# Performance work log

Hardware: AMD Instinct MI355X
Metric: run time of the kernel (lower is better)

Reference implementation:

```python
import jax, jax.numpy as jnp
import numpy as np

B, T, IN, PRE, LH, NH, ACT_H, NPOL, NVAL = 32, 512, 256, 512, 512, 1024, 512, 64, 1


def setup_inputs() -> dict:
    key = jax.random.key(0)
    ks = jax.random.split(key, 10)
    def w(k, shape, fan_in):
        return jax.random.normal(k, shape, jnp.float32) / np.sqrt(fan_in).astype(np.float32)
    return {
        "x": jax.random.normal(ks[0], (B, T, IN), jnp.float32),
        "pre_W0": w(ks[1], (PRE, IN), IN), "pre_b0": jnp.zeros((PRE,), jnp.float32),
        "pre_W1": w(ks[2], (LH, PRE), PRE), "pre_b1": jnp.zeros((LH,), jnp.float32),
        "weight_ih": w(ks[3], (4 * NH, LH), LH), "weight_hh": w(ks[4], (4 * NH, NH), NH),
        "bias_ih": jnp.zeros((4 * NH,), jnp.float32), "bias_hh": jnp.zeros((4 * NH,), jnp.float32),
        "act_W0": w(ks[5], (ACT_H, NH), NH), "act_b0": jnp.zeros((ACT_H,), jnp.float32),
        "act_W1": w(ks[6], (NPOL, ACT_H), ACT_H), "act_b1": jnp.zeros((NPOL,), jnp.float32),
        "val_W0": w(ks[7], (ACT_H, NH), NH), "val_b0": jnp.zeros((ACT_H,), jnp.float32),
        "val_W1": w(ks[8], (NVAL, ACT_H), ACT_H), "val_b1": jnp.zeros((NVAL,), jnp.float32),
    }


def reference(x, pre_W0, pre_b0, pre_W1, pre_b1, weight_ih, weight_hh, bias_ih, bias_hh,
              act_W0, act_b0, act_W1, act_b1, val_W0, val_b0, val_W1, val_b1):
    # pre_dnn: relu hidden layer + linear output ('linear')
    h = jnp.maximum(x @ pre_W0.T + pre_b0, 0.0)
    u = h @ pre_W1.T + pre_b1                         # [B,T,LH]
    # SeqLSTM: torch lstm_cell semantics (gate order i,f,g,o), zero initial (h,c)
    # precompute input contribution to gates outside the scan
    x_gates = u @ weight_ih.T + (bias_ih + bias_hh)   # [B,T,4H]
    x_gates = jnp.swapaxes(x_gates, 0, 1)             # [T,B,4H]
    H = weight_hh.shape[1]

    def step(carry, gx):
        hh, cc = carry
        gates = gx + hh @ weight_hh.T
        i, f, g, o = jnp.split(gates, 4, axis=-1)
        cc = jax.nn.sigmoid(f) * cc + jax.nn.sigmoid(i) * jnp.tanh(g)
        hh = jax.nn.sigmoid(o) * jnp.tanh(cc)
        return (hh, cc), hh

    init = (jnp.zeros((x.shape[0], H), x.dtype), jnp.zeros((x.shape[0], H), x.dtype))
    _, hs = jax.lax.scan(step, init, x_gates)         # hs: [T,B,H]
    hs = jnp.swapaxes(hs, 0, 1)                       # [B,T,H]
    # act_dnn ('softmax') and val_dnn ('linear') on all hidden states
    a = jnp.maximum(hs @ act_W0.T + act_b0, 0.0)
    probs = jax.nn.softmax(a @ act_W1.T + act_b1, axis=-1)   # [B,T,NPOL]
    v = jnp.maximum(hs @ val_W0.T + val_b0, 0.0)
    value = v @ val_W1.T + val_b1                              # [B,T,NVAL]
    return probs, value
```

## Files before the change

### kernel.cpp

```cpp
#include <hip/hip_runtime.h>
#include <stdint.h>

#define TT 512
#define NB 32

typedef __attribute__((ext_vector_type(8))) short bf16x8;
typedef __attribute__((ext_vector_type(4))) float f32x4;

#define O_XB   0ull
#define O_W0   8388608ull
#define O_W1   8650752ull
#define O_WIH  9175040ull
#define O_WHH  13369344ull
#define O_WA0  21757952ull
#define O_WA1  22806528ull
#define O_WV0  22872064ull
#define O_WV1  23920640ull
#define O_GB   23921664ull
#define O_H1   23938048ull
#define O_U    40715264ull
#define O_GX   57492480ull
#define O_HS   191710208ull
#define O_HBUF 225264640ull
#define O_FLG  225395712ull
#define WS_NEED 225399808ull

__device__ __forceinline__ unsigned short f2bf(float f) {
  unsigned u = __builtin_bit_cast(unsigned, f);
  u = (u + 0x7fffu + ((u >> 16) & 1u)) >> 16;
  return (unsigned short)u;
}
__device__ __forceinline__ float bf2f(unsigned short h) {
  unsigned u = ((unsigned)h) << 16;
  return __builtin_bit_cast(float, u);
}
__device__ __forceinline__ float bf2f_lo(unsigned w) { return __builtin_bit_cast(float, w << 16); }
__device__ __forceinline__ float bf2f_hi(unsigned w) { return __builtin_bit_cast(float, w & 0xffff0000u); }

__device__ __forceinline__ float dot8(uint4 a, uint4 b, float acc) {
  acc = fmaf(bf2f_lo(a.x), bf2f_lo(b.x), acc);
  acc = fmaf(bf2f_hi(a.x), bf2f_hi(b.x), acc);
  acc = fmaf(bf2f_lo(a.y), bf2f_lo(b.y), acc);
  acc = fmaf(bf2f_hi(a.y), bf2f_hi(b.y), acc);
  acc = fmaf(bf2f_lo(a.z), bf2f_lo(b.z), acc);
  acc = fmaf(bf2f_hi(a.z), bf2f_hi(b.z), acc);
  acc = fmaf(bf2f_lo(a.w), bf2f_lo(b.w), acc);
  acc = fmaf(bf2f_hi(a.w), bf2f_hi(b.w), acc);
  return acc;
}
__device__ __forceinline__ float sigf(float x) { return 1.f / (1.f + __expf(-x)); }
__device__ __forceinline__ float tanhf_(float x) { float e = __expf(2.f * x); return 1.f - 2.f / (e + 1.f); }

__global__ void cvt_kernel(const float* __restrict__ x,  const float* __restrict__ w0,
                           const float* __restrict__ w1, const float* __restrict__ wih,
                           const float* __restrict__ whh, const float* __restrict__ wa0,
                           const float* __restrict__ wa1, const float* __restrict__ wv0,
                           const float* __restrict__ wv1, const float* __restrict__ bih,
                           const float* __restrict__ bhh, unsigned char* __restrict__ ws) {
  unsigned i = blockIdx.x * 256u + threadIdx.x;
  if (i >= 2991232u) return;
  const float* s; unsigned long long off; unsigned local;
  if      (i < 1048576u) { s = x;   off = O_XB;  local = i; }
  else if (i < 1081344u) { s = w0;  off = O_W0;  local = i - 1048576u; }
  else if (i < 1146880u) { s = w1;  off = O_W1;  local = i - 1081344u; }
  else if (i < 1671168u) { s = wih; off = O_WIH; local = i - 1146880u; }
  else if (i < 2719744u) { s = whh; off = O_WHH; local = i - 1671168u; }
  else if (i < 2850816u) { s = wa0; off = O_WA0; local = i - 2719744u; }
  else if (i < 2859008u) { s = wa1; off = O_WA1; local = i - 2850816u; }
  else if (i < 2990080u) { s = wv0; off = O_WV0; local = i - 2859008u; }
  else if (i < 2990208u) { s = wv1; off = O_WV1; local = i - 2990080u; }
  else {
    unsigned l2 = i - 2990208u;
    float4 a = ((const float4*)bih)[l2];
    float4 b = ((const float4*)bhh)[l2];
    float4 o; o.x = a.x + b.x; o.y = a.y + b.y; o.z = a.z + b.z; o.w = a.w + b.w;
    ((float4*)(ws + O_GB))[l2] = o;
    return;
  }
  float4 v = ((const float4*)s)[local];
  ushort4 o; o.x = f2bf(v.x); o.y = f2bf(v.y); o.z = f2bf(v.z); o.w = f2bf(v.w);
  ((ushort4*)(ws + off))[local] = o;
}

template<int RELU, int ILV>
__global__ __launch_bounds__(256, 2) void gemm_bt(const unsigned short* __restrict__ A,
    const unsigned short* __restrict__ Bw, const float* __restrict__ bias,
    unsigned short* __restrict__ C, int M, int N, int K) {
  __shared__ unsigned short As[128 * 40];
  __shared__ unsigned short Bs[128 * 40];
  const int tid = threadIdx.x;
  const int l = tid & 63, w = tid >> 6;
  const int wm = (w >> 1) * 64, wn = (w & 1) * 64;
  const int m0 = blockIdx.y * 128, n0 = blockIdx.x * 128;
  const int sr = tid >> 2;
  const int sk = (tid & 3) * 8;
  const int fr = l & 15;
  const int kf = (l >> 4) * 8;
  f32x4 acc[4][4] = {};
  for (int kb = 0; kb < K; kb += 32) {
    uint4 a0 = *(const uint4*)(A + (size_t)(m0 + sr) * K + kb + sk);
    uint4 a1 = *(const uint4*)(A + (size_t)(m0 + sr + 64) * K + kb + sk);
    uint4 b0 = *(const uint4*)(Bw + (size_t)(n0 + sr) * K + kb + sk);
    uint4 b1 = *(const uint4*)(Bw + (size_t)(n0 + sr + 64) * K + kb + sk);
    __syncthreads();
    *(uint4*)(As + sr * 40 + sk) = a0;
    *(uint4*)(As + (sr + 64) * 40 + sk) = a1;
    *(uint4*)(Bs + sr * 40 + sk) = b0;
    *(uint4*)(Bs + (sr + 64) * 40 + sk) = b1;
    __syncthreads();
    bf16x8 af[4], bfr[4];
    #pragma unroll
    for (int mt = 0; mt < 4; mt++)
      af[mt] = __builtin_bit_cast(bf16x8, *(const uint4*)(As + (wm + mt * 16 + fr) * 40 + kf));
    #pragma unroll
    for (int nt = 0; nt < 4; nt++)
      bfr[nt] = __builtin_bit_cast(bf16x8, *(const uint4*)(Bs + (wn + nt * 16 + fr) * 40 + kf));
    #pragma unroll
    for (int mt = 0; mt < 4; mt++)
      #pragma unroll
      for (int nt = 0; nt < 4; nt++)
        acc[mt][nt] = __builtin_amdgcn_mfma_f32_16x16x32_bf16(af[mt], bfr[nt], acc[mt][nt], 0, 0, 0);
  }
  const int rq = (l >> 4) * 4;
  #pragma unroll
  for (int nt = 0; nt < 4; nt++) {
    int n = n0 + wn + nt * 16 + fr;
    float bv = bias[n];
    #pragma unroll
    for (int mt = 0; mt < 4; mt++) {
      int rb = m0 + wm + mt * 16 + rq;
      #pragma unroll
      for (int i = 0; i < 4; i++) {
        float v = acc[mt][nt][i] + bv;
        if (RELU) v = fmaxf(v, 0.f);
        int r = rb + i;
        size_t orow = ILV ? ((size_t)(r & (TT - 1)) * NB + (size_t)(r >> 9)) : (size_t)r;
        C[orow * (size_t)N + n] = f2bf(v);
      }
    }
  }
}

__global__ __launch_bounds__(256, 1) void lstm_scan(
    const unsigned short* __restrict__ whh,
    const unsigned short* __restrict__ gx,
    unsigned short* __restrict__ hbuf,
    unsigned short* __restrict__ hs,
    unsigned int* __restrict__ flags) {
  __shared__ float part[4096];
  const int tid = threadIdx.x;
  const int l = tid & 63, w = tid >> 6;
  const int g = blockIdx.x >> 6;
  const int s = blockIdx.x & 63;
  const int fr = l & 15, kf = (l >> 4) * 8;

  bf16x8 wf[4][8];
  #pragma unroll
  for (int q = 0; q < 4; q++)
    #pragma unroll
    for (int ks = 0; ks < 8; ks++) {
      int row = q * 1024 + s * 16 + fr;
      int k = w * 256 + ks * 32 + kf;
      wf[q][ks] = __builtin_bit_cast(bf16x8, *(const uint4*)(whh + (size_t)row * 1024 + k));
    }

  const int pm = tid >> 3;
  const int j2 = (tid & 7) * 2;
  float c0 = 0.f, c1 = 0.f;
  unsigned int* myflag = flags + (size_t)(g * 64 + s) * 8;
  const unsigned int* pollp = flags + (size_t)(g * 64 + l) * 8;

  for (int t = 0; t < TT; t++) {
    unsigned gxw0 = 0, gxw1 = 0, gxw2 = 0, gxw3 = 0;
    if (tid < 128) {
      const unsigned* gp = (const unsigned*)(gx + ((size_t)t * NB + g * 16 + pm) * 4096 + s * 16 + j2);
      gxw0 = gp[0]; gxw1 = gp[512]; gxw2 = gp[1024]; gxw3 = gp[1536];
    }
    if (t > 0 && w == 0) {
      while (true) {
        unsigned f = __hip_atomic_load(pollp, __ATOMIC_RELAXED, __HIP_MEMORY_SCOPE_AGENT);
        if (!__any((int)(f < (unsigned)t))) break;
        __builtin_amdgcn_s_sleep(1);
      }
    }
    __syncthreads();
    asm volatile("" ::: "memory");

    const unsigned short* hb = hbuf + (size_t)(g * 2 + (t & 1)) * 16384;
    const unsigned long long* hq = (const unsigned long long*)(hb + (size_t)fr * 1024);
    bf16x8 hf[8];
    #pragma unroll
    for (int ks = 0; ks < 8; ks++) {
      int k4 = (w * 256 + ks * 32 + kf) >> 2;
      unsigned long long lo = __hip_atomic_load(hq + k4,     __ATOMIC_RELAXED, __HIP_MEMORY_SCOPE_AGENT);
      unsigned long long hi = __hip_atomic_load(hq + k4 + 1, __ATOMIC_RELAXED, __HIP_MEMORY_SCOPE_AGENT);
      uint4 u; u.x = (unsigned)lo; u.y = (unsigned)(lo >> 32);
      u.z = (unsigned)hi; u.w = (unsigned)(hi >> 32);
      hf[ks] = __builtin_bit_cast(bf16x8, u);
    }
    f32x4 acc[4] = {};
    #pragma unroll
    for (int ks = 0; ks < 8; ks++)
      #pragma unroll
      for (int q = 0; q < 4; q++)
        acc[q] = __builtin_amdgcn_mfma_f32_16x16x32_bf16(hf[ks], wf[q][ks], acc[q], 0, 0, 0);
    #pragma unroll
    for (int q = 0; q < 4; q++)
      *(f32x4*)(&part[((w * 4 + q) * 64 + l) * 4]) = acc[q];
    __syncthreads();

    if (tid < 128) {
      const int lane0 = (pm >> 2) * 16 + j2;
      const int reg = pm & 3;
      unsigned gxw[4] = {gxw0, gxw1, gxw2, gxw3};
      float gv[4][2];
      #pragma unroll
      for (int q = 0; q < 4; q++) {
        float v0 = bf2f_lo(gxw[q]);
        float v1 = bf2f_hi(gxw[q]);
        #pragma unroll
        for (int ww = 0; ww < 4; ww++) {
          v0 += part[((ww * 4 + q) * 64 + lane0) * 4 + reg];
          v1 += part[((ww * 4 + q) * 64 + lane0 + 1) * 4 + reg];
        }
        gv[q][0] = v0; gv[q][1] = v1;
      }
      float si0 = sigf(gv[0][0]), si1 = sigf(gv[0][1]);
      float sf0 = sigf(gv[1][0]), sf1 = sigf(gv[1][1]);
      float tg0 = tanhf_(gv[2][0]), tg1 = tanhf_(gv[2][1]);
      float so0 = sigf(gv[3][0]), so1 = sigf(gv[3][1]);
      c0 = sf0 * c0 + si0 * tg0;
      c1 = sf1 * c1 + si1 * tg1;
      float h0 = so0 * tanhf_(c0);
      float h1 = so1 * tanhf_(c1);
      unsigned hv = (unsigned)f2bf(h0) | ((unsigned)f2bf(h1) << 16);
      unsigned short* hn = hbuf + (size_t)(g * 2 + ((t + 1) & 1)) * 16384;
      __hip_atomic_store((unsigned*)(hn + (size_t)pm * 1024 + s * 16 + j2), hv,
                         __ATOMIC_RELAXED, __HIP_MEMORY_SCOPE_AGENT);
      *(unsigned*)(hs + ((size_t)(g * 16 + pm) * TT + t) * 1024 + s * 16 + j2) = hv;
      asm volatile("s_waitcnt vmcnt(0)" ::: "memory");
    }
    __syncthreads();
    if (tid == 0)
      __hip_atomic_store(myflag, (unsigned)(t + 1), __ATOMIC_RELAXED, __HIP_MEMORY_SCOPE_AGENT);
  }
}

__global__ __launch_bounds__(512, 1) void act1_softmax(const unsigned short* __restrict__ Aa,
    const unsigned short* __restrict__ W1, const float* __restrict__ b1,
    float* __restrict__ out) {
  __shared__ unsigned short wl[64 * 512];
  const int tid = threadIdx.x;
  #pragma unroll
  for (int r = 0; r < 8; r++) {
    int e = r * 512 + tid;
    int col = e >> 6, kc = e & 63;
    *(uint4*)(wl + ((size_t)kc * 64 + col) * 8) = *(const uint4*)(W1 + (size_t)col * 512 + kc * 8);
  }
  __syncthreads();
  const int l = tid & 63, w = tid >> 6;
  size_t row = (size_t)blockIdx.x * 8 + w;
  const unsigned short* ar = Aa + row * 512;
  float acc = 0.f;
  for (int kc = 0; kc < 64; kc++) {
    uint4 au = *(const uint4*)(ar + kc * 8);
    uint4 wu = *(const uint4*)(wl + ((size_t)kc * 64 + l) * 8);
    acc = dot8(au, wu, acc);
  }
  float logit = acc + b1[l];
  float mx = logit;
  #pragma unroll
  for (int off = 32; off >= 1; off >>= 1) mx = fmaxf(mx, __shfl_xor(mx, off));
  float e = __expf(logit - mx);
  float ssum = e;
  #pragma unroll
  for (int off = 32; off >= 1; off >>= 1) ssum += __shfl_xor(ssum, off);
  out[row * 64 + l] = e / ssum;
}

__global__ __launch_bounds__(256, 4) void val1_kernel(const unsigned short* __restrict__ V,
    const unsigned short* __restrict__ w1, const float* __restrict__ b1,
    float* __restrict__ out) {
  const int tid = threadIdx.x;
  const int l = tid & 63, w = tid >> 6;
  size_t row = (size_t)blockIdx.x * 4 + w;
  uint4 vu = *(const uint4*)(V + row * 512 + l * 8);
  uint4 wu = *(const uint4*)(w1 + l * 8);
  float s = dot8(vu, wu, 0.f);
  #pragma unroll
  for (int off = 32; off >= 1; off >>= 1) s += __shfl_xor(s, off);
  if (l == 0) out[1048576u + row] = s + b1[0];
}

extern "C" void kernel_launch(void* const* d_in, const int* in_sizes, int n_in,
                              void* d_out, int out_size, void* d_ws, size_t ws_size,
                              hipStream_t stream) {
  (void)in_sizes; (void)n_in; (void)out_size;
  if (ws_size < WS_NEED) return;
  const float* x   = (const float*)d_in[0];
  const float* pw0 = (const float*)d_in[1];
  const float* pb0 = (const float*)d_in[2];
  const float* pw1 = (const float*)d_in[3];
  const float* pb1 = (const float*)d_in[4];
  const float* wih = (const float*)d_in[5];
  const float* whh = (const float*)d_in[6];
  const float* bih = (const float*)d_in[7];
  const float* bhh = (const float*)d_in[8];
  const float* aw0 = (const float*)d_in[9];
  const float* ab0 = (const float*)d_in[10];
  const float* aw1 = (const float*)d_in[11];
  const float* ab1 = (const float*)d_in[12];
  const float* vw0 = (const float*)d_in[13];
  const float* vb0 = (const float*)d_in[14];
  const float* vw1 = (const float*)d_in[15];
  const float* vb1 = (const float*)d_in[16];
  unsigned char* ws = (unsigned char*)d_ws;
  float* out = (float*)d_out;

  const unsigned short* xb   = (const unsigned short*)(ws + O_XB);
  const unsigned short* w0b  = (const unsigned short*)(ws + O_W0);
  const unsigned short* w1b  = (const unsigned short*)(ws + O_W1);
  const unsigned short* wihb = (const unsigned short*)(ws + O_WIH);
  const unsigned short* whhb = (const unsigned short*)(ws + O_WHH);
  const unsigned short* wa0b = (const unsigned short*)(ws + O_WA0);
  const unsigned short* wa1b = (const unsigned short*)(ws + O_WA1);
  const unsigned short* wv0b = (const unsigned short*)(ws + O_WV0);
  const unsigned short* wv1b = (const unsigned short*)(ws + O_WV1);
  const float* gbp = (const float*)(ws + O_GB);
  unsigned short* h1b = (unsigned short*)(ws + O_H1);
  unsigned short* ub  = (unsigned short*)(ws + O_U);
  unsigned short* gxb = (unsigned short*)(ws + O_GX);
  unsigned short* hsb = (unsigned short*)(ws + O_HS);
  unsigned short* hbufp = (unsigned short*)(ws + O_HBUF);
  unsigned int* flgp = (unsigned int*)(ws + O_FLG);
  unsigned short* aab = h1b;
  unsigned short* vvb = ub;

  hipMemsetAsync(ws + O_HBUF, 0, 131072 + 4096, stream);
  cvt_kernel<<<11685, 256, 0, stream>>>(x, pw0, pw1, wih, whh, aw0, aw1, vw0, vw1, bih, bhh, ws);
  gemm_bt<1, 0><<<dim3(4, 128), 256, 0, stream>>>(xb, w0b, pb0, h1b, 16384, 512, 256);
  gemm_bt<0, 0><<<dim3(4, 128), 256, 0, stream>>>(h1b, w1b, pb1, ub, 16384, 512, 512);
  gemm_bt<0, 1><<<dim3(32, 128), 256, 0, stream>>>(ub, wihb, gbp, gxb, 16384, 4096, 512);
  {
    const unsigned short* a_whh = whhb;
    const unsigned short* a_gx  = gxb;
    unsigned short* a_hbuf = hbufp;
    unsigned short* a_hs   = hsb;
    unsigned int*   a_flg  = flgp;
    void* args[5] = { (void*)&a_whh, (void*)&a_gx, (void*)&a_hbuf, (void*)&a_hs, (void*)&a_flg };
    hipLaunchCooperativeKernel((void*)lstm_scan, dim3(128), dim3(256), args, 0, stream);
  }
  gemm_bt<1, 0><<<dim3(4, 128), 256, 0, stream>>>(hsb, wa0b, ab0, aab, 16384, 512, 1024);
  gemm_bt<1, 0><<<dim3(4, 128), 256, 0, stream>>>(hsb, wv0b, vb0, vvb, 16384, 512, 1024);
  act1_softmax<<<2048, 512, 0, stream>>>(aab, wa1b, ab1, out);
  val1_kernel<<<4096, 256, 0, stream>>>(vvb, wv1b, vb1, out);
}
```

Before: 2.530 ms.

## Replace per-block flags with step-tagged hidden-state packets in LSTM scan

The recurrent scan no longer uses per-block flag words polled by one wave followed by barriers. Each bf16 hidden value is now stored in a 32-bit word whose upper half carries the timestep tag. Consumers spin on the data itself until every tag matches, so the flag store, the vmcnt wait and one block barrier per step go away. The cost is twice the bytes for hidden-state exchange and every wave polling its own data. The buffer is also moved into the reused H1 region, with the memset placed after the GEMMs.

New measurement: 4.464 ms. +76.4%, slower.

```diff
diff --git a/kernel.cpp b/kernel.cpp
--- a/kernel.cpp
+++ b/kernel.cpp
@@ -21,18 +21,12 @@
 #define O_U    40715264ull
 #define O_GX   57492480ull
 #define O_HS   191710208ull
-#define O_HBUF 225264640ull
-#define O_FLG  225395712ull
-#define WS_NEED 225399808ull
+#define WS_NEED 225264640ull
 
 __device__ __forceinline__ unsigned short f2bf(float f) {
   unsigned u = __builtin_bit_cast(unsigned, f);
   u = (u + 0x7fffu + ((u >> 16) & 1u)) >> 16;
   return (unsigned short)u;
-}
-__device__ __forceinline__ float bf2f(unsigned short h) {
-  unsigned u = ((unsigned)h) << 16;
-  return __builtin_bit_cast(float, u);
 }
 __device__ __forceinline__ float bf2f_lo(unsigned w) { return __builtin_bit_cast(float, w << 16); }
 __device__ __forceinline__ float bf2f_hi(unsigned w) { return __builtin_bit_cast(float, w & 0xffff0000u); }
@@ -144,9 +138,8 @@
 __global__ __launch_bounds__(256, 1) void lstm_scan(
     const unsigned short* __restrict__ whh,
     const unsigned short* __restrict__ gx,
-    unsigned short* __restrict__ hbuf,
-    unsigned short* __restrict__ hs,
-    unsigned int* __restrict__ flags) {
+    unsigned* __restrict__ pk,
+    unsigned short* __restrict__ hs) {
   __shared__ float part[4096];
   const int tid = threadIdx.x;
   const int l = tid & 63, w = tid >> 6;
@@ -166,9 +159,8 @@
 
   const int pm = tid >> 3;
   const int j2 = (tid & 7) * 2;
+  const int kh = w * 128 + (kf >> 1);
   float c0 = 0.f, c1 = 0.f;
-  unsigned int* myflag = flags + (size_t)(g * 64 + s) * 8;
-  const unsigned int* pollp = flags + (size_t)(g * 64 + l) * 8;
 
   for (int t = 0; t < TT; t++) {
     unsigned gxw0 = 0, gxw1 = 0, gxw2 = 0, gxw3 = 0;
@@ -176,27 +168,38 @@
       const unsigned* gp = (const unsigned*)(gx + ((size_t)t * NB + g * 16 + pm) * 4096 + s * 16 + j2);
       gxw0 = gp[0]; gxw1 = gp[512]; gxw2 = gp[1024]; gxw3 = gp[1536];
     }
-    if (t > 0 && w == 0) {
-      while (true) {
-        unsigned f = __hip_atomic_load(pollp, __ATOMIC_RELAXED, __HIP_MEMORY_SCOPE_AGENT);
-        if (!__any((int)(f < (unsigned)t))) break;
-        __builtin_amdgcn_s_sleep(1);
+
+    const unsigned long long* hq =
+        (const unsigned long long*)(pk + (((size_t)(g * 2 + (t & 1)) * 16 + fr) << 10));
+    unsigned long long raw[32];
+    const unsigned expv = ((unsigned)t) << 16;
+    while (true) {
+      #pragma unroll
+      for (int ks = 0; ks < 8; ks++)
+        #pragma unroll
+        for (int j = 0; j < 4; j++)
+          raw[ks * 4 + j] = __hip_atomic_load(hq + kh + ks * 16 + j,
+                                              __ATOMIC_RELAXED, __HIP_MEMORY_SCOPE_AGENT);
+      unsigned mism = 0;
+      #pragma unroll
+      for (int i = 0; i < 32; i++) {
+        unsigned lo = (unsigned)raw[i];
+        unsigned hi = (unsigned)(raw[i] >> 32);
+        mism |= ((lo ^ expv) | (hi ^ expv)) & 0xffff0000u;
       }
-    }
-    __syncthreads();
-    asm volatile("" ::: "memory");
-
-    const unsigned short* hb = hbuf + (size_t)(g * 2 + (t & 1)) * 16384;
-    const unsigned long long* hq = (const unsigned long long*)(hb + (size_t)fr * 1024);
+      if (!__any((int)(mism != 0u))) break;
+      __builtin_amdgcn_s_sleep(1);
+    }
+
     bf16x8 hf[8];
     #pragma unroll
     for (int ks = 0; ks < 8; ks++) {
-      int k4 = (w * 256 + ks * 32 + kf) >> 2;
-      unsigned long long lo = __hip_atomic_load(hq + k4,     __ATOMIC_RELAXED, __HIP_MEMORY_SCOPE_AGENT);
-      unsigned long long hi = __hip_atomic_load(hq + k4 + 1, __ATOMIC_RELAXED, __HIP_MEMORY_SCOPE_AGENT);
-      uint4 u; u.x = (unsigned)lo; u.y = (unsigned)(lo >> 32);
-      u.z = (unsigned)hi; u.w = (unsigned)(hi >> 32);
-      hf[ks] = __builtin_bit_cast(bf16x8, u);
+      #pragma unroll
+      for (int j = 0; j < 4; j++) {
+        unsigned long long r_ = raw[ks * 4 + j];
+        hf[ks][2 * j]     = (short)(unsigned short)(r_ & 0xffffu);
+        hf[ks][2 * j + 1] = (short)(unsigned short)((r_ >> 32) & 0xffffu);
+      }
     }
     f32x4 acc[4] = {};
     #pragma unroll
@@ -204,6 +207,7 @@
       #pragma unroll
       for (int q = 0; q < 4; q++)
         acc[q] = __builtin_amdgcn_mfma_f32_16x16x32_bf16(hf[ks], wf[q][ks], acc[q], 0, 0, 0);
+    __syncthreads();
     #pragma unroll
     for (int q = 0; q < 4; q++)
       *(f32x4*)(&part[((w * 4 + q) * 64 + l) * 4]) = acc[q];
@@ -233,16 +237,16 @@
       c1 = sf1 * c1 + si1 * tg1;
       float h0 = so0 * tanhf_(c0);
       float h1 = so1 * tanhf_(c1);
-      unsigned hv = (unsigned)f2bf(h0) | ((unsigned)f2bf(h1) << 16);
-      unsigned short* hn = hbuf + (size_t)(g * 2 + ((t + 1) & 1)) * 16384;
-      __hip_atomic_store((unsigned*)(hn + (size_t)pm * 1024 + s * 16 + j2), hv,
-                         __ATOMIC_RELAXED, __HIP_MEMORY_SCOPE_AGENT);
-      *(unsigned*)(hs + ((size_t)(g * 16 + pm) * TT + t) * 1024 + s * 16 + j2) = hv;
-      asm volatile("s_waitcnt vmcnt(0)" ::: "memory");
-    }
-    __syncthreads();
-    if (tid == 0)
-      __hip_atomic_store(myflag, (unsigned)(t + 1), __ATOMIC_RELAXED, __HIP_MEMORY_SCOPE_AGENT);
+      unsigned hb0 = (unsigned)f2bf(h0), hb1 = (unsigned)f2bf(h1);
+      unsigned tagw = ((unsigned)(t + 1)) << 16;
+      unsigned long long pkt = (unsigned long long)(hb0 | tagw) |
+                               ((unsigned long long)(hb1 | tagw) << 32);
+      unsigned long long* dst = (unsigned long long*)(
+          pk + (((size_t)(g * 2 + ((t + 1) & 1)) * 16 + pm) << 10) + s * 16 + j2);
+      __hip_atomic_store(dst, pkt, __ATOMIC_RELAXED, __HIP_MEMORY_SCOPE_AGENT);
+      *(unsigned*)(hs + ((size_t)(g * 16 + pm) * TT + t) * 1024 + s * 16 + j2) =
+          hb0 | (hb1 << 16);
+    }
   }
 }
 
@@ -331,23 +335,21 @@
   unsigned short* ub  = (unsigned short*)(ws + O_U);
   unsigned short* gxb = (unsigned short*)(ws + O_GX);
   unsigned short* hsb = (unsigned short*)(ws + O_HS);
-  unsigned short* hbufp = (unsigned short*)(ws + O_HBUF);
-  unsigned int* flgp = (unsigned int*)(ws + O_FLG);
+  unsigned* pkb = (unsigned*)(ws + O_H1);
   unsigned short* aab = h1b;
   unsigned short* vvb = ub;
 
-  hipMemsetAsync(ws + O_HBUF, 0, 131072 + 4096, stream);
   cvt_kernel<<<11685, 256, 0, stream>>>(x, pw0, pw1, wih, whh, aw0, aw1, vw0, vw1, bih, bhh, ws);
   gemm_bt<1, 0><<<dim3(4, 128), 256, 0, stream>>>(xb, w0b, pb0, h1b, 16384, 512, 256);
   gemm_bt<0, 0><<<dim3(4, 128), 256, 0, stream>>>(h1b, w1b, pb1, ub, 16384, 512, 512);
   gemm_bt<0, 1><<<dim3(32, 128), 256, 0, stream>>>(ub, wihb, gbp, gxb, 16384, 4096, 512);
+  hipMemsetAsync(ws + O_H1, 0, 4 * 16 * 1024 * 4, stream);
   {
     const unsigned short* a_whh = whhb;
     const unsigned short* a_gx  = gxb;
-    unsigned short* a_hbuf = hbufp;
-    unsigned short* a_hs   = hsb;
-    unsigned int*   a_flg  = flgp;
-    void* args[5] = { (void*)&a_whh, (void*)&a_gx, (void*)&a_hbuf, (void*)&a_hs, (void*)&a_flg };
+    unsigned*       a_pk = pkb;
+    unsigned short* a_hs = hsb;
+    void* args[4] = { (void*)&a_whh, (void*)&a_gx, (void*)&a_pk, (void*)&a_hs };
     hipLaunchCooperativeKernel((void*)lstm_scan, dim3(128), dim3(256), args, 0, stream);
   }
   gemm_bt<1, 0><<<dim3(4, 128), 256, 0, stream>>>(hsb, wa0b, ab0, aab, 16384, 512, 1024);
```

## Store LSTM hidden state in MFMA fragment order and defer hs write

Applied to the files above, without the earlier changes.

The exchange buffer for h between scan blocks is rearranged into the MFMA operand fragment layout, so each lane reads its fragment with contiguous coalesced 16-byte loads instead of strided row reads. The hs history store is moved after the flag publish, taking it off the critical path of the per-step barrier. The h buffer and flags now reuse the dead h1 workspace region, cleared just before the scan. This requires more complex index math on the producer side and relies on the h1 region being unused while the scan runs.

Measured after the change: 2.350 ms. -7.1%, faster.

```diff
diff --git a/kernel.cpp b/kernel.cpp
--- a/kernel.cpp
+++ b/kernel.cpp
@@ -21,18 +21,12 @@
 #define O_U    40715264ull
 #define O_GX   57492480ull
 #define O_HS   191710208ull
-#define O_HBUF 225264640ull
-#define O_FLG  225395712ull
-#define WS_NEED 225399808ull
+#define WS_NEED 225264640ull
 
 __device__ __forceinline__ unsigned short f2bf(float f) {
   unsigned u = __builtin_bit_cast(unsigned, f);
   u = (u + 0x7fffu + ((u >> 16) & 1u)) >> 16;
   return (unsigned short)u;
-}
-__device__ __forceinline__ float bf2f(unsigned short h) {
-  unsigned u = ((unsigned)h) << 16;
-  return __builtin_bit_cast(float, u);
 }
 __device__ __forceinline__ float bf2f_lo(unsigned w) { return __builtin_bit_cast(float, w << 16); }
 __device__ __forceinline__ float bf2f_hi(unsigned w) { return __builtin_bit_cast(float, w & 0xffff0000u); }
@@ -144,9 +138,8 @@
 __global__ __launch_bounds__(256, 1) void lstm_scan(
     const unsigned short* __restrict__ whh,
     const unsigned short* __restrict__ gx,
-    unsigned short* __restrict__ hbuf,
-    unsigned short* __restrict__ hs,
-    unsigned int* __restrict__ flags) {
+    unsigned* __restrict__ pk,
+    unsigned short* __restrict__ hs) {
   __shared__ float part[4096];
   const int tid = threadIdx.x;
   const int l = tid & 63, w = tid >> 6;
@@ -166,9 +159,18 @@
 
   const int pm = tid >> 3;
   const int j2 = (tid & 7) * 2;
+  const int D0  = s * 16 + j2;
+  const int pw  = D0 >> 8;
+  const int pr  = D0 & 255;
+  const int pks = pr >> 5;
+  const int pkfg= (pr & 31) >> 3;
+  const int pjj = (pr & 7) >> 1;
+  const unsigned pidx = ((unsigned)((pw * 8 + pks) * 64 + pkfg * 16 + pm) << 2) + pjj;
+
+  unsigned* flags = pk + 32768;
+  unsigned* myflag = flags + (size_t)(g * 64 + s) * 8;
+  const unsigned* pollp = flags + (size_t)(g * 64 + l) * 8;
   float c0 = 0.f, c1 = 0.f;
-  unsigned int* myflag = flags + (size_t)(g * 64 + s) * 8;
-  const unsigned int* pollp = flags + (size_t)(g * 64 + l) * 8;
 
   for (int t = 0; t < TT; t++) {
     unsigned gxw0 = 0, gxw1 = 0, gxw2 = 0, gxw3 = 0;
@@ -186,14 +188,14 @@
     __syncthreads();
     asm volatile("" ::: "memory");
 
-    const unsigned short* hb = hbuf + (size_t)(g * 2 + (t & 1)) * 16384;
-    const unsigned long long* hq = (const unsigned long long*)(hb + (size_t)fr * 1024);
+    const unsigned long long* hq =
+        (const unsigned long long*)(pk + (size_t)(g * 2 + (t & 1)) * 8192);
     bf16x8 hf[8];
     #pragma unroll
     for (int ks = 0; ks < 8; ks++) {
-      int k4 = (w * 256 + ks * 32 + kf) >> 2;
-      unsigned long long lo = __hip_atomic_load(hq + k4,     __ATOMIC_RELAXED, __HIP_MEMORY_SCOPE_AGENT);
-      unsigned long long hi = __hip_atomic_load(hq + k4 + 1, __ATOMIC_RELAXED, __HIP_MEMORY_SCOPE_AGENT);
+      size_t i2 = ((size_t)(w * 8 + ks) * 64 + l) * 2;
+      unsigned long long lo = __hip_atomic_load(hq + i2,     __ATOMIC_RELAXED, __HIP_MEMORY_SCOPE_AGENT);
+      unsigned long long hi = __hip_atomic_load(hq + i2 + 1, __ATOMIC_RELAXED, __HIP_MEMORY_SCOPE_AGENT);
       uint4 u; u.x = (unsigned)lo; u.y = (unsigned)(lo >> 32);
       u.z = (unsigned)hi; u.w = (unsigned)(hi >> 32);
       hf[ks] = __builtin_bit_cast(bf16x8, u);
@@ -209,6 +211,7 @@
       *(f32x4*)(&part[((w * 4 + q) * 64 + l) * 4]) = acc[q];
     __syncthreads();
 
+    unsigned hb01 = 0;
     if (tid < 128) {
       const int lane0 = (pm >> 2) * 16 + j2;
       const int reg = pm & 3;
@@ -233,16 +236,16 @@
       c1 = sf1 * c1 + si1 * tg1;
       float h0 = so0 * tanhf_(c0);
       float h1 = so1 * tanhf_(c1);
-      unsigned hv = (unsigned)f2bf(h0) | ((unsigned)f2bf(h1) << 16);
-      unsigned short* hn = hbuf + (size_t)(g * 2 + ((t + 1) & 1)) * 16384;
-      __hip_atomic_store((unsigned*)(hn + (size_t)pm * 1024 + s * 16 + j2), hv,
-                         __ATOMIC_RELAXED, __HIP_MEMORY_SCOPE_AGENT);
-      *(unsigned*)(hs + ((size_t)(g * 16 + pm) * TT + t) * 1024 + s * 16 + j2) = hv;
+      hb01 = (unsigned)f2bf(h0) | ((unsigned)f2bf(h1) << 16);
+      unsigned* dst = pk + (size_t)(g * 2 + ((t + 1) & 1)) * 8192 + pidx;
+      __hip_atomic_store(dst, hb01, __ATOMIC_RELAXED, __HIP_MEMORY_SCOPE_AGENT);
       asm volatile("s_waitcnt vmcnt(0)" ::: "memory");
     }
     __syncthreads();
     if (tid == 0)
       __hip_atomic_store(myflag, (unsigned)(t + 1), __ATOMIC_RELAXED, __HIP_MEMORY_SCOPE_AGENT);
+    if (tid < 128)
+      *(unsigned*)(hs + ((size_t)(g * 16 + pm) * TT + t) * 1024 + s * 16 + j2) = hb01;
   }
 }
 
@@ -331,23 +334,21 @@
   unsigned short* ub  = (unsigned short*)(ws + O_U);
   unsigned short* gxb = (unsigned short*)(ws + O_GX);
   unsigned short* hsb = (unsigned short*)(ws + O_HS);
-  unsigned short* hbufp = (unsigned short*)(ws + O_HBUF);
-  unsigned int* flgp = (unsigned int*)(ws + O_FLG);
+  unsigned* pkb = (unsigned*)(ws + O_H1);
   unsigned short* aab = h1b;
   unsigned short* vvb = ub;
 
-  hipMemsetAsync(ws + O_HBUF, 0, 131072 + 4096, stream);
   cvt_kernel<<<11685, 256, 0, stream>>>(x, pw0, pw1, wih, whh, aw0, aw1, vw0, vw1, bih, bhh, ws);
   gemm_bt<1, 0><<<dim3(4, 128), 256, 0, stream>>>(xb, w0b, pb0, h1b, 16384, 512, 256);
   gemm_bt<0, 0><<<dim3(4, 128), 256, 0, stream>>>(h1b, w1b, pb1, ub, 16384, 512, 512);
   gemm_bt<0, 1><<<dim3(32, 128), 256, 0, stream>>>(ub, wihb, gbp, gxb, 16384, 4096, 512);
+  hipMemsetAsync(ws + O_H1, 0, 135168, stream);
   {
     const unsigned short* a_whh = whhb;
     const unsigned short* a_gx  = gxb;
-    unsigned short* a_hbuf = hbufp;
-    unsigned short* a_hs   = hsb;
-    unsigned int*   a_flg  = flgp;
-    void* args[5] = { (void*)&a_whh, (void*)&a_gx, (void*)&a_hbuf, (void*)&a_hs, (void*)&a_flg };
+    unsigned*       a_pk = pkb;
+    unsigned short* a_hs = hsb;
+    void* args[4] = { (void*)&a_whh, (void*)&a_gx, (void*)&a_pk, (void*)&a_hs };
     hipLaunchCooperativeKernel((void*)lstm_scan, dim3(128), dim3(256), args, 0, stream);
   }
   gemm_bt<1, 0><<<dim3(4, 128), 256, 0, stream>>>(hsb, wa0b, ab0, aab, 16384, 512, 1024);
```
